# Kernel tuning notes

Measured on AMD Instinct MI355X. Metric: run time of the kernel, lower is better.

The kernel has to match this reference:

```python
import jax, jax.numpy as jnp
import numpy as np

B = 4096        # graphs
N0 = 32         # nodes per graph
N = B * N0      # 131072 nodes
EP = 128        # edges per graph
E = B * EP      # 524288 edges
H, C = 2, 64    # heads, per-head channels
D = H * C       # 128
K1, K2, K3 = 29, 27, 25  # ceil(0.9*32), ceil(0.9*29), ceil(0.9*27)


def setup_inputs() -> dict:
    key = jax.random.key(0)
    ks = jax.random.split(key, 8)
    x = jax.random.normal(ks[0], (N, 41), jnp.float32)
    g = jnp.repeat(jnp.arange(B, dtype=jnp.int32), EP)
    src = g * N0 + jax.random.randint(ks[1], (E,), 0, N0, jnp.int32)
    dst = g * N0 + jax.random.randint(ks[2], (E,), 0, N0, jnp.int32)
    edge_index = jnp.stack([src, dst])
    edge_attr = jax.random.normal(ks[3], (E, 10), jnp.float32)
    batch = jnp.repeat(jnp.arange(B, dtype=jnp.int32), N0)

    def lin(k, i, o):
        return jax.random.normal(k, (i, o), jnp.float32) / np.float32(np.sqrt(i))

    p = {"x": x, "edge_index": edge_index, "edge_attr": edge_attr, "batch": batch}
    fins = {1: 41, 2: D, 3: D}
    for li in (1, 2, 3):
        sub = jax.random.split(ks[3 + li], 6)
        p[f"W{li}"] = lin(sub[0], fins[li], D)
        p[f"We{li}"] = lin(sub[1], 10, D)
        p[f"as{li}"] = jax.random.normal(sub[2], (H, C), jnp.float32) * 0.1
        p[f"ad{li}"] = jax.random.normal(sub[3], (H, C), jnp.float32) * 0.1
        p[f"ae{li}"] = jax.random.normal(sub[4], (H, C), jnp.float32) * 0.1
        p[f"b{li}"] = jnp.zeros((D,), jnp.float32)
        p[f"g{li}"] = jnp.ones((D,), jnp.float32)
        p[f"be{li}"] = jnp.zeros((D,), jnp.float32)
        p[f"pw{li}"] = jax.random.normal(sub[5], (D,), jnp.float32)
    sub = jax.random.split(ks[7], 2)
    p["fw1"] = lin(sub[0], D, 64)
    p["fb1"] = jnp.zeros((64,), jnp.float32)
    p["fw2"] = lin(sub[1], 64, 1)
    p["fb2"] = jnp.zeros((1,), jnp.float32)
    return p


def gat_conv(x, src, dst, edge_attr, node_mask, edge_mask, W, We, a_s, a_d, a_e, b):
    # PyG GATConv w/ edge_dim, add_self_loops=True, fill_value='mean'
    emf = edge_mask.astype(x.dtype)
    loop_attr = jax.ops.segment_sum(edge_attr * emf[:, None], dst, num_segments=N)
    loop_attr = loop_attr / jnp.maximum(jax.ops.segment_sum(emf, dst, num_segments=N), 1.0)[:, None]
    idx = jnp.arange(N, dtype=src.dtype)
    s = jnp.concatenate([src, idx])
    d = jnp.concatenate([dst, idx])
    ea = jnp.concatenate([edge_attr, loop_attr], axis=0)
    msk = jnp.concatenate([edge_mask, node_mask])
    h = (x @ W).reshape(N, H, C)                       # [N,H,C]
    eh = (ea @ We).reshape(-1, H, C)                   # [E+N,H,C]
    alpha = (h * a_s).sum(-1)[s] + (h * a_d).sum(-1)[d] + (eh * a_e).sum(-1)
    alpha = jax.nn.leaky_relu(alpha, 0.2)              # [E+N,H]
    alpha = jnp.where(msk[:, None], alpha, -1e9)
    mx = jax.ops.segment_max(alpha, d, num_segments=N)  # segment softmax over dst
    p = jnp.where(msk[:, None], jnp.exp(alpha - mx[d]), 0.0)
    den = jax.ops.segment_sum(p, d, num_segments=N)
    w = p / jnp.maximum(den[d], 1e-16)
    out = jax.ops.segment_sum(w[:, :, None] * h[s], d, num_segments=N)
    return out.reshape(N, D) + b


def masked_bn(x, nm, gamma, beta, eps=1e-5):
    m = nm.astype(x.dtype)[:, None]
    n = jnp.maximum(m.sum(), 1.0)
    mu = (x * m).sum(0) / n
    var = (jnp.square(x - mu) * m).sum(0) / n
    return gamma * (x - mu) * jax.lax.rsqrt(var + eps) + beta


def topk_pool(x, w, nm, k):
    sc = (x @ w) / jnp.linalg.norm(w)                  # [N]
    sg = jnp.where(nm, sc, -1e9).reshape(B, N0)
    _, idx = jax.lax.top_k(sg, k)                      # per-graph top-k
    nm2 = jnp.zeros((B, N0), bool).at[jnp.arange(B)[:, None], idx].set(True).reshape(-1)
    xn = jnp.where(nm2[:, None], x * jnp.tanh(sc)[:, None], 0.0)
    return xn, nm2


def graph_mean(x, nm, batch):
    m = nm.astype(x.dtype)
    s = jax.ops.segment_sum(x * m[:, None], batch, num_segments=B)
    c = jax.ops.segment_sum(m, batch, num_segments=B)
    return s / jnp.maximum(c, 1.0)[:, None]


def _forward(x, edge_index, edge_attr, batch,
             W1, We1, as1, ad1, ae1, b1, g1, be1, pw1,
             W2, We2, as2, ad2, ae2, b2, g2, be2, pw2,
             W3, We3, as3, ad3, ae3, b3, g3, be3, pw3,
             fw1, fb1, fw2, fb2):
    src, dst = edge_index[0], edge_index[1]
    nm = jnp.ones((N,), bool)
    em = jnp.ones((E,), bool)
    layers = [(W1, We1, as1, ad1, ae1, b1, g1, be1, pw1, K1),
              (W2, We2, as2, ad2, ae2, b2, g2, be2, pw2, K2),
              (W3, We3, as3, ad3, ae3, b3, g3, be3, pw3, K3)]
    reads = []
    for (W, We, a_s, a_d, a_e, b, g, be, pw, k) in layers:
        x = gat_conv(x, src, dst, edge_attr, nm, em, W, We, a_s, a_d, a_e, b)
        x = jax.nn.relu(masked_bn(x, nm, g, be))
        x, nm = topk_pool(x, pw, nm, k)
        em = em & nm[src] & nm[dst]
        reads.append(graph_mean(x, nm, batch))
    z = reads[0] + reads[1] + reads[2]
    z = jax.nn.relu(z @ fw1 + fb1)
    return z @ fw2 + fb2


def reference(x, edge_index, edge_attr, batch,
              W1, We1, as1, ad1, ae1, b1, g1, be1, pw1,
              W2, We2, as2, ad2, ae2, b2, g2, be2, pw2,
              W3, We3, as3, ad3, ae3, b3, g3, be3, pw3,
              fw1, fb1, fw2, fb2):
    return _forward(x, edge_index, edge_attr, batch,
                    W1, We1, as1, ad1, ae1, b1, g1, be1, pw1,
                    W2, We2, as2, ad2, ae2, b2, g2, be2, pw2,
                    W3, We3, as3, ad3, ae3, b3, g3, be3, pw3,
                    fw1, fb1, fw2, fb2)
```

## Files before the change

### kernel.cpp

```cpp
#include <hip/hip_runtime.h>

#define NN 131072
#define NG 4096
#define NE 524288

__device__ __forceinline__ float lrelu(float a){ return a>=0.f ? a : 0.2f*a; }

template<int K, int PMODE, int KSEL>
__global__ __launch_bounds__(256) void pool_gemm_kernel(
    const float* __restrict__ Xin, float* bufA, unsigned char* nmg,
    const float* __restrict__ stat,
    const float* __restrict__ gamma, const float* __restrict__ beta,
    const float* __restrict__ Wg,
    float* zacc)
{
    constexpr int XP = (K == 41) ? 44 : 132;
    __shared__ float xs[64 * XP];
    __shared__ float scS[64], tsS[64];
    __shared__ int   nmlS[64];

    int tid = threadIdx.x;
    long row0 = (long)blockIdx.x * 64;
    int g0 = blockIdx.x * 2;

    if (PMODE == 0) {
        for (int i = tid; i < 64 * 41; i += 256) {
            int r = i / 41, c = i - r * 41;
            xs[r * 44 + c] = Xin[row0 * 41 + i];
        }
    } else {
        for (int i = tid; i < 2048; i += 256) {
            int r = i >> 5, dc = (i & 31) * 4;
            float4 v = *(const float4*)&bufA[(row0 + r) * 128 + dc];
            v.x = fmaxf(gamma[dc    ] * (v.x - stat[dc    ]) * stat[128 + dc    ] + beta[dc    ], 0.f);
            v.y = fmaxf(gamma[dc + 1] * (v.y - stat[dc + 1]) * stat[128 + dc + 1] + beta[dc + 1], 0.f);
            v.z = fmaxf(gamma[dc + 2] * (v.z - stat[dc + 2]) * stat[128 + dc + 2] + beta[dc + 2], 0.f);
            v.w = fmaxf(gamma[dc + 3] * (v.w - stat[dc + 3]) * stat[128 + dc + 3] + beta[dc + 3], 0.f);
            *(float4*)&xs[r * XP + dc] = v;
        }
        if (tid < 64) nmlS[tid] = (PMODE == 1) ? 1 : (int)nmg[g0 * 32 + tid];
    }
    __syncthreads();

    if (PMODE > 0) {
        {
            int node = tid >> 2, l4 = tid & 3;
            float s = 0.f;
            for (int m = 0; m < 32; m++) { int c = l4 + 4 * m; s += xs[node * XP + c] * stat[256 + c]; }
            s += __shfl_xor(s, 2); s += __shfl_xor(s, 1);
            if (l4 == 0) scS[node] = s;
        }
        __syncthreads();
        if (tid < 64) {
            int gp = tid >> 5, n = tid & 31;
            float sn = nmlS[tid] ? scS[tid] : -1e9f;
            int cnt = 0;
            for (int j = 0; j < 32; j++) {
                float sj = nmlS[gp * 32 + j] ? scS[gp * 32 + j] : -1e9f;
                cnt += (sj > sn || (sj == sn && j < n)) ? 1 : 0;
            }
            int sl = (cnt < KSEL) ? 1 : 0;
            nmg[g0 * 32 + tid] = (unsigned char)sl;
            tsS[tid] = sl ? tanhf(scS[tid]) : 0.f;
        }
        __syncthreads();
        for (int i = tid; i < 2048; i += 256) {
            int r = i >> 5, dc = (i & 31) * 4;
            float t = tsS[r];
            float4 v = *(const float4*)&xs[r * XP + dc];
            v.x *= t; v.y *= t; v.z *= t; v.w *= t;
            *(float4*)&xs[r * XP + dc] = v;
        }
        __syncthreads();
        {
            int gp = tid >> 7, d = tid & 127;
            float s = 0.f;
            for (int n = 0; n < 32; n++) s += xs[(gp * 32 + n) * XP + d];
            zacc[(long)(g0 + gp) * 128 + d] += s * (1.0f / (float)KSEL);
        }
        __syncthreads();
    }

    int r0 = (tid >> 5) * 8, c4 = (tid & 31) * 4;
    float acc[8][4];
#pragma unroll
    for (int i = 0; i < 8; i++)
#pragma unroll
        for (int j = 0; j < 4; j++) acc[i][j] = 0.f;

    constexpr int KM4 = (K / 4) * 4;
#pragma unroll 2
    for (int k0 = 0; k0 < KM4; k0 += 4) {
        float4 wv0 = *(const float4*)&Wg[(k0 + 0) * 128 + c4];
        float4 wv1 = *(const float4*)&Wg[(k0 + 1) * 128 + c4];
        float4 wv2 = *(const float4*)&Wg[(k0 + 2) * 128 + c4];
        float4 wv3 = *(const float4*)&Wg[(k0 + 3) * 128 + c4];
#pragma unroll
        for (int i = 0; i < 8; i++) {
            float4 xv = *(const float4*)&xs[(r0 + i) * XP + k0];
            acc[i][0] += xv.x * wv0.x + xv.y * wv1.x + xv.z * wv2.x + xv.w * wv3.x;
            acc[i][1] += xv.x * wv0.y + xv.y * wv1.y + xv.z * wv2.y + xv.w * wv3.y;
            acc[i][2] += xv.x * wv0.z + xv.y * wv1.z + xv.z * wv2.z + xv.w * wv3.z;
            acc[i][3] += xv.x * wv0.w + xv.y * wv1.w + xv.z * wv2.w + xv.w * wv3.w;
        }
    }
    for (int k = KM4; k < K; k++) {
        float4 wv = *(const float4*)&Wg[k * 128 + c4];
#pragma unroll
        for (int i = 0; i < 8; i++) {
            float xv = xs[(r0 + i) * XP + k];
            acc[i][0] += xv * wv.x; acc[i][1] += xv * wv.y;
            acc[i][2] += xv * wv.z; acc[i][3] += xv * wv.w;
        }
    }
#pragma unroll
    for (int i = 0; i < 8; i++)
        *(float4*)&bufA[(row0 + r0 + i) * 128 + c4] =
            make_float4(acc[i][0], acc[i][1], acc[i][2], acc[i][3]);
}

__global__ __launch_bounds__(256) void attn_kernel(
    float* bufA,
    const int* __restrict__ srcp, const int* __restrict__ dstp,
    const float* __restrict__ EA,
    const unsigned char* __restrict__ nmg,
    const float* __restrict__ stat,
    const float* __restrict__ as_, const float* __restrict__ ad_,
    const float* __restrict__ bb,
    float* sums)
{
    __shared__ float hs[32 * 128];
    __shared__ float Wm[2 * 32 * 36];
    __shared__ float scr[320];
    __shared__ unsigned char nmlS[32];

    int g = blockIdx.x, tid = threadIdx.x;
    long gb = (long)g * 4096;

    float ea0 = 0.f, ea1 = 0.f;
    int myls = 0, myld = 0;
    if (tid < 128) {
        myls = srcp[g * 128 + tid] & 31;
        myld = dstp[g * 128 + tid] & 31;
        const float* ep = EA + (long)(g * 128 + tid) * 10;
#pragma unroll
        for (int j = 0; j < 10; j++) { float v = ep[j]; ea0 += v * stat[384 + j]; ea1 += v * stat[394 + j]; }
    }
    for (int i = tid; i < 2304; i += 256) Wm[i] = 0.f;
    if (tid < 96) scr[128 + tid] = 0.f;
    if (tid < 32) nmlS[tid] = nmg[g * 32 + tid];
#pragma unroll
    for (int k = 0; k < 4; k++) {
        int i = tid + 256 * k, r = i >> 5, c4 = i & 31;
        *(float4*)&hs[r * 128 + ((c4 ^ (r & 7)) << 2)] =
            *(const float4*)&bufA[gb + (long)i * 4];
    }
    __syncthreads();

    {
        int node = tid >> 3, l8 = tid & 7, rb = node * 128, k = node & 7;
        float s0 = 0, s1 = 0, d0 = 0, d1 = 0;
#pragma unroll
        for (int m = 0; m < 8; m++) {
            int c = l8 + 8 * m, c4 = c >> 2, j = c & 3;
            int o0 = rb + ((c4 ^ k) << 2) + j;
            float h0 = hs[o0], h1 = hs[o0 + 64];
            s0 += h0 * as_[c];      s1 += h1 * as_[64 + c];
            d0 += h0 * ad_[c];      d1 += h1 * ad_[64 + c];
        }
        s0 += __shfl_xor(s0, 4); s0 += __shfl_xor(s0, 2); s0 += __shfl_xor(s0, 1);
        s1 += __shfl_xor(s1, 4); s1 += __shfl_xor(s1, 2); s1 += __shfl_xor(s1, 1);
        d0 += __shfl_xor(d0, 4); d0 += __shfl_xor(d0, 2); d0 += __shfl_xor(d0, 1);
        d1 += __shfl_xor(d1, 4); d1 += __shfl_xor(d1, 2); d1 += __shfl_xor(d1, 1);
        if (l8 == 0) {
            scr[node * 2] = s0;      scr[node * 2 + 1] = s1;
            scr[64 + node * 2] = d0; scr[64 + node * 2 + 1] = d1;
        }
    }
    int mymk = 0;
    if (tid < 128) {
        mymk = (int)nmlS[myls] & (int)nmlS[myld];
        if (mymk) {
            atomicAdd(&scr[128 + myld * 2], ea0);
            atomicAdd(&scr[128 + myld * 2 + 1], ea1);
            atomicAdd(&scr[192 + myld], 1.f);
        }
    }
    __syncthreads();

    if (tid < 128) {
        if (mymk) {
            float p0 = __expf(lrelu(scr[myls * 2]     + scr[64 + myld * 2]     + ea0));
            float p1 = __expf(lrelu(scr[myls * 2 + 1] + scr[64 + myld * 2 + 1] + ea1));
            atomicAdd(&Wm[myls * 36 + myld], p0);
            atomicAdd(&Wm[1152 + myls * 36 + myld], p1);
        }
    } else if (tid < 192) {
        int t2 = tid - 128, n = t2 >> 1, h = t2 & 1;
        if (nmlS[n]) {
            float c = scr[192 + n]; c = (c > 0.f) ? c : 1.f;
            float ps = __expf(lrelu(scr[n * 2 + h] + scr[64 + n * 2 + h] + scr[128 + n * 2 + h] / c));
            atomicAdd(&Wm[h * 1152 + n * 36 + n], ps);
        }
    }
    __syncthreads();

    if (tid < 64) {
        int n = tid & 31, h = tid >> 5;
        const float* Wh = &Wm[h * 1152 + n];
        float den = 0.f;
#pragma unroll 8
        for (int s = 0; s < 32; s++) den += Wh[s * 36];
        scr[256 + h * 32 + n] = 1.f / fmaxf(den, 1e-16f);
    } else if (tid < 128) {
        *(float4*)&scr[(tid - 64) * 4] = make_float4(0.f, 0.f, 0.f, 0.f);
    }
    __syncthreads();

    {
        int d = tid & 127, h = d >> 6, nb = tid >> 7;
        int c4 = d >> 2, j = d & 3;
        const float* Wh = &Wm[h * 1152 + nb * 16];
        float acc[16];
#pragma unroll
        for (int i = 0; i < 16; i++) acc[i] = 0.f;
        for (int s = 0; s < 32; s++) {
            float hv = hs[s * 128 + ((c4 ^ (s & 7)) << 2) + j];
            float4 w0 = *(const float4*)&Wh[s * 36];
            float4 w1 = *(const float4*)&Wh[s * 36 + 4];
            float4 w2 = *(const float4*)&Wh[s * 36 + 8];
            float4 w3 = *(const float4*)&Wh[s * 36 + 12];
            acc[0]  += w0.x * hv; acc[1]  += w0.y * hv; acc[2]  += w0.z * hv; acc[3]  += w0.w * hv;
            acc[4]  += w1.x * hv; acc[5]  += w1.y * hv; acc[6]  += w1.z * hv; acc[7]  += w1.w * hv;
            acc[8]  += w2.x * hv; acc[9]  += w2.y * hv; acc[10] += w2.z * hv; acc[11] += w2.w * hv;
            acc[12] += w3.x * hv; acc[13] += w3.y * hv; acc[14] += w3.z * hv; acc[15] += w3.w * hv;
        }
        float bv = bb[d];
        float sp = 0.f, sq = 0.f;
#pragma unroll
        for (int i = 0; i < 16; i++) {
            int n = nb * 16 + i;
            float v = acc[i] * scr[256 + h * 32 + n] + bv;
            bufA[gb + n * 128 + d] = v;
            if (nmlS[n]) { sp += v; sq += v * v; }
        }
        atomicAdd(&scr[d], sp);
        atomicAdd(&scr[128 + d], sq);
    }
    __syncthreads();

    if (tid < 128) {
        int rep = (g & 31) * 256;
        atomicAdd(&sums[rep + tid], scr[tid]);
        atomicAdd(&sums[rep + 128 + tid], scr[128 + tid]);
    }
}

__global__ __launch_bounds__(128) void setup_kernel(
    float* sums, float* stat, const float* __restrict__ We, const float* __restrict__ ae)
{
    int t = threadIdx.x;
    for (int i = t; i < 32 * 256; i += 128) sums[i] = 0.f;
    if (t < 20) {
        int h = t / 10, j = t - 10 * h;
        float s = 0.f;
        for (int c = 0; c < 64; c++) s += We[j * 128 + h * 64 + c] * ae[h * 64 + c];
        stat[384 + t] = s;
    }
}

__global__ __launch_bounds__(128) void finalize_kernel(
    float* sums, float n, const float* __restrict__ pw, float* stat,
    const float* __restrict__ Wen, const float* __restrict__ aen)
{
    int d = threadIdx.x;
    float s1 = 0.f, s2 = 0.f;
#pragma unroll
    for (int r = 0; r < 32; r++) { s1 += sums[r * 256 + d]; s2 += sums[r * 256 + 128 + d]; }
    float mean = s1 / n;
    float var = s2 / n - mean * mean;
    if (var < 0.f) var = 0.f;
    float rstd = rsqrtf(var + 1e-5f);
    float p = pw[d];
    float q = p * p;
#pragma unroll
    for (int o = 32; o >= 1; o >>= 1) q += __shfl_xor(q, o);
    __shared__ float w2[2];
    if ((d & 63) == 0) w2[d >> 6] = q;
    __syncthreads();
    float nrm = sqrtf(w2[0] + w2[1]);
    stat[d] = mean; stat[128 + d] = rstd; stat[256 + d] = p / nrm;
    if (d < 20) {
        int h = d / 10, j = d - 10 * h;
        float s = 0.f;
        for (int c = 0; c < 64; c++) s += Wen[j * 128 + h * 64 + c] * aen[h * 64 + c];
        stat[384 + d] = s;
    }
    for (int i = d; i < 32 * 256; i += 128) sums[i] = 0.f;
}

__global__ __launch_bounds__(256) void final_kernel(
    const float* __restrict__ bufA, const unsigned char* __restrict__ nmg,
    const float* __restrict__ stat,
    const float* __restrict__ gamma, const float* __restrict__ beta,
    const float* __restrict__ zacc,
    const float* __restrict__ fw1, const float* __restrict__ fb1,
    const float* __restrict__ fw2, const float* __restrict__ fb2,
    float* __restrict__ out)
{
    __shared__ float xs[32 * 132], zt[128], hred[64], scS[32], tsS[32];
    __shared__ int nmlS[32];
    int g = blockIdx.x, tid = threadIdx.x;
    long gb = (long)g * 4096;

    if (tid < 32) nmlS[tid] = (int)nmg[g * 32 + tid];
    for (int i = tid; i < 1024; i += 256) {
        int r = i >> 5, dc = (i & 31) * 4;
        float4 v = *(const float4*)&bufA[gb + i * 4];
        v.x = fmaxf(gamma[dc    ] * (v.x - stat[dc    ]) * stat[128 + dc    ] + beta[dc    ], 0.f);
        v.y = fmaxf(gamma[dc + 1] * (v.y - stat[dc + 1]) * stat[128 + dc + 1] + beta[dc + 1], 0.f);
        v.z = fmaxf(gamma[dc + 2] * (v.z - stat[dc + 2]) * stat[128 + dc + 2] + beta[dc + 2], 0.f);
        v.w = fmaxf(gamma[dc + 3] * (v.w - stat[dc + 3]) * stat[128 + dc + 3] + beta[dc + 3], 0.f);
        *(float4*)&xs[r * 132 + dc] = v;
    }
    __syncthreads();

    {
        int node = tid >> 3, l8 = tid & 7;
        float s = 0.f;
        for (int m = 0; m < 16; m++) { int c = l8 + 8 * m; s += xs[node * 132 + c] * stat[256 + c]; }
        s += __shfl_xor(s, 4); s += __shfl_xor(s, 2); s += __shfl_xor(s, 1);
        if (l8 == 0) scS[node] = s;
    }
    __syncthreads();

    if (tid < 32) {
        float sn = nmlS[tid] ? scS[tid] : -1e9f;
        int cnt = 0;
        for (int j = 0; j < 32; j++) {
            float sj = nmlS[j] ? scS[j] : -1e9f;
            cnt += (sj > sn || (sj == sn && j < tid)) ? 1 : 0;
        }
        tsS[tid] = (cnt < 25) ? tanhf(scS[tid]) : 0.f;
    }
    __syncthreads();

    if (tid < 128) {
        float s = 0.f;
        for (int n = 0; n < 32; n++) s += xs[n * 132 + tid] * tsS[n];
        zt[tid] = zacc[(long)g * 128 + tid] + s * (1.0f / 25.0f);
    }
    __syncthreads();

    {
        int j = tid >> 2, p = tid & 3;
        float s = 0.f;
        for (int d = p * 32; d < p * 32 + 32; d++) s += zt[d] * fw1[d * 64 + j];
        s += __shfl_xor(s, 1); s += __shfl_xor(s, 2);
        if (p == 0) hred[j] = fmaxf(s + fb1[j], 0.f) * fw2[j];
    }
    __syncthreads();
    if (tid < 64) {
        float v = hred[tid];
#pragma unroll
        for (int o = 32; o >= 1; o >>= 1) v += __shfl_xor(v, o);
        if (tid == 0) out[g] = v + fb2[0];
    }
}

extern "C" void kernel_launch(void* const* d_in, const int* in_sizes, int n_in,
                              void* d_out, int out_size, void* d_ws, size_t ws_size,
                              hipStream_t stream)
{
    const float* X0 = (const float*)d_in[0];
    const int*   EI = (const int*)d_in[1];
    const float* EA = (const float*)d_in[2];
    const int* srcp = EI;
    const int* dstp = EI + NE;

    const float* W1  = (const float*)d_in[4];  const float* We1 = (const float*)d_in[5];
    const float* as1 = (const float*)d_in[6];  const float* ad1 = (const float*)d_in[7];
    const float* ae1 = (const float*)d_in[8];  const float* b1  = (const float*)d_in[9];
    const float* g1  = (const float*)d_in[10]; const float* be1 = (const float*)d_in[11];
    const float* pw1 = (const float*)d_in[12];
    const float* W2  = (const float*)d_in[13]; const float* We2 = (const float*)d_in[14];
    const float* as2 = (const float*)d_in[15]; const float* ad2 = (const float*)d_in[16];
    const float* ae2 = (const float*)d_in[17]; const float* b2  = (const float*)d_in[18];
    const float* g2  = (const float*)d_in[19]; const float* be2 = (const float*)d_in[20];
    const float* pw2 = (const float*)d_in[21];
    const float* W3  = (const float*)d_in[22]; const float* We3 = (const float*)d_in[23];
    const float* as3 = (const float*)d_in[24]; const float* ad3 = (const float*)d_in[25];
    const float* ae3 = (const float*)d_in[26]; const float* b3  = (const float*)d_in[27];
    const float* g3  = (const float*)d_in[28]; const float* be3 = (const float*)d_in[29];
    const float* pw3 = (const float*)d_in[30];
    const float* fw1 = (const float*)d_in[31]; const float* fb1 = (const float*)d_in[32];
    const float* fw2 = (const float*)d_in[33]; const float* fb2 = (const float*)d_in[34];

    float* bufA = (float*)d_ws;
    float* z    = bufA + (size_t)NN * 128;
    float* sums = z + (size_t)NG * 128;
    float* stat = sums + 32 * 256;
    unsigned char* nmg = (unsigned char*)(stat + 512);

    hipMemsetAsync(nmg, 1, NN, stream);
    hipMemsetAsync(z, 0, (size_t)NG * 128 * sizeof(float), stream);
    setup_kernel<<<1, 128, 0, stream>>>(sums, stat, We1, ae1);

    pool_gemm_kernel<41, 0, 1><<<NN / 64, 256, 0, stream>>>(
        X0, bufA, nmg, stat, g1, be1, W1, z);
    attn_kernel<<<NG, 256, 0, stream>>>(bufA, srcp, dstp, EA, nmg, stat, as1, ad1, b1, sums);
    finalize_kernel<<<1, 128, 0, stream>>>(sums, 131072.f, pw1, stat, We2, ae2);

    pool_gemm_kernel<128, 1, 29><<<NN / 64, 256, 0, stream>>>(
        X0, bufA, nmg, stat, g1, be1, W2, z);
    attn_kernel<<<NG, 256, 0, stream>>>(bufA, srcp, dstp, EA, nmg, stat, as2, ad2, b2, sums);
    finalize_kernel<<<1, 128, 0, stream>>>(sums, 4096.f * 29.f, pw2, stat, We3, ae3);

    pool_gemm_kernel<128, 2, 27><<<NN / 64, 256, 0, stream>>>(
        X0, bufA, nmg, stat, g2, be2, W3, z);
    attn_kernel<<<NG, 256, 0, stream>>>(bufA, srcp, dstp, EA, nmg, stat, as3, ad3, b3, sums);
    finalize_kernel<<<1, 128, 0, stream>>>(sums, 4096.f * 27.f, pw3, stat, We3, ae3);

    final_kernel<<<NG, 256, 0, stream>>>(
        bufA, nmg, stat, g3, be3, z, fw1, fb1, fw2, fb2, (float*)d_out);
}
```

Baseline: 533.8 us.

## Fuse pool/GEMM and attention kernels into one per-layer kernel

Merges the pooling+linear-projection kernel with the GAT attention/aggregation kernel so each block of 64 nodes (two graphs) projects features into shared memory and then performs attention and aggregation without writing and rereading the projected features through global memory. The shared feature tile is switched to an XOR-swizzled 128-wide layout, and the attention stage now handles two graphs per block. This removes one kernel launch per layer and a full round trip of the node feature buffer, at the cost of higher shared memory use per block (about 56KB), which may lower occupancy.

```diff
diff --git a/kernel.cpp b/kernel.cpp
--- a/kernel.cpp
+++ b/kernel.cpp
@@ -7,21 +7,42 @@
 __device__ __forceinline__ float lrelu(float a){ return a>=0.f ? a : 0.2f*a; }
 
 template<int K, int PMODE, int KSEL>
-__global__ __launch_bounds__(256) void pool_gemm_kernel(
+__global__ __launch_bounds__(256) void layer_kernel(
     const float* __restrict__ Xin, float* bufA, unsigned char* nmg,
     const float* __restrict__ stat,
     const float* __restrict__ gamma, const float* __restrict__ beta,
     const float* __restrict__ Wg,
-    float* zacc)
+    float* zacc,
+    const int* __restrict__ srcp, const int* __restrict__ dstp,
+    const float* __restrict__ EA,
+    const float* __restrict__ as_, const float* __restrict__ ad_,
+    const float* __restrict__ bb,
+    float* sums)
 {
-    constexpr int XP = (K == 41) ? 44 : 132;
-    __shared__ float xs[64 * XP];
+    __shared__ float xs[64 * 128];
+    __shared__ float Wm[4608];
+    __shared__ float scr[576];
     __shared__ float scS[64], tsS[64];
-    __shared__ int   nmlS[64];
+    __shared__ unsigned char nmlS[64];
 
     int tid = threadIdx.x;
     long row0 = (long)blockIdx.x * 64;
     int g0 = blockIdx.x * 2;
+
+    int eid = g0 * 128 + tid;
+    int myls = srcp[eid] & 31, myld = dstp[eid] & 31;
+    int gph = tid >> 7;
+    int ls64 = gph * 32 + myls, ld64 = gph * 32 + myld;
+    float ea0 = 0.f, ea1 = 0.f;
+    {
+        const float* ep = EA + (long)eid * 10;
+#pragma unroll
+        for (int j = 0; j < 10; j++) { float v = ep[j]; ea0 += v * stat[384 + j]; ea1 += v * stat[394 + j]; }
+    }
+
+    for (int i = tid; i < 4608; i += 256) Wm[i] = 0.f;
+    if (tid < 192) scr[256 + tid] = 0.f;
+    if (tid < 64) nmlS[tid] = (PMODE == 2) ? nmg[g0 * 32 + tid] : (unsigned char)1;
 
     if (PMODE == 0) {
         for (int i = tid; i < 64 * 41; i += 256) {
@@ -30,27 +51,28 @@
         }
     } else {
         for (int i = tid; i < 2048; i += 256) {
-            int r = i >> 5, dc = (i & 31) * 4;
+            int r = i >> 5, c4 = i & 31, dc = c4 * 4;
             float4 v = *(const float4*)&bufA[(row0 + r) * 128 + dc];
             v.x = fmaxf(gamma[dc    ] * (v.x - stat[dc    ]) * stat[128 + dc    ] + beta[dc    ], 0.f);
             v.y = fmaxf(gamma[dc + 1] * (v.y - stat[dc + 1]) * stat[128 + dc + 1] + beta[dc + 1], 0.f);
             v.z = fmaxf(gamma[dc + 2] * (v.z - stat[dc + 2]) * stat[128 + dc + 2] + beta[dc + 2], 0.f);
             v.w = fmaxf(gamma[dc + 3] * (v.w - stat[dc + 3]) * stat[128 + dc + 3] + beta[dc + 3], 0.f);
-            *(float4*)&xs[r * XP + dc] = v;
-        }
-        if (tid < 64) nmlS[tid] = (PMODE == 1) ? 1 : (int)nmg[g0 * 32 + tid];
+            *(float4*)&xs[r * 128 + ((c4 ^ (r & 7)) << 2)] = v;
+        }
     }
     __syncthreads();
 
     if (PMODE > 0) {
         {
-            int node = tid >> 2, l4 = tid & 3;
+            int node = tid >> 2, l4 = tid & 3, kk = node & 7;
             float s = 0.f;
-            for (int m = 0; m < 32; m++) { int c = l4 + 4 * m; s += xs[node * XP + c] * stat[256 + c]; }
+            for (int m = 0; m < 32; m++)
+                s += xs[node * 128 + (((m ^ kk)) << 2) + l4] * stat[256 + 4 * m + l4];
             s += __shfl_xor(s, 2); s += __shfl_xor(s, 1);
             if (l4 == 0) scS[node] = s;
         }
         __syncthreads();
+        int sl = 0;
         if (tid < 64) {
             int gp = tid >> 5, n = tid & 31;
             float sn = nmlS[tid] ? scS[tid] : -1e9f;
@@ -59,29 +81,35 @@
                 float sj = nmlS[gp * 32 + j] ? scS[gp * 32 + j] : -1e9f;
                 cnt += (sj > sn || (sj == sn && j < n)) ? 1 : 0;
             }
-            int sl = (cnt < KSEL) ? 1 : 0;
+            sl = (cnt < KSEL) ? 1 : 0;
+        }
+        __syncthreads();
+        if (tid < 64) {
             nmg[g0 * 32 + tid] = (unsigned char)sl;
+            nmlS[tid] = (unsigned char)sl;
             tsS[tid] = sl ? tanhf(scS[tid]) : 0.f;
         }
         __syncthreads();
         for (int i = tid; i < 2048; i += 256) {
-            int r = i >> 5, dc = (i & 31) * 4;
+            int r = i >> 5, c4 = i & 31;
             float t = tsS[r];
-            float4 v = *(const float4*)&xs[r * XP + dc];
+            float4* p = (float4*)&xs[r * 128 + ((c4 ^ (r & 7)) << 2)];
+            float4 v = *p;
             v.x *= t; v.y *= t; v.z *= t; v.w *= t;
-            *(float4*)&xs[r * XP + dc] = v;
+            *p = v;
         }
         __syncthreads();
         {
-            int gp = tid >> 7, d = tid & 127;
+            int gp = tid >> 7, d = tid & 127, c4 = d >> 2, j = d & 3;
             float s = 0.f;
-            for (int n = 0; n < 32; n++) s += xs[(gp * 32 + n) * XP + d];
+            for (int n = 0; n < 32; n++)
+                s += xs[(gp * 32 + n) * 128 + ((c4 ^ (n & 7)) << 2) + j];
             zacc[(long)(g0 + gp) * 128 + d] += s * (1.0f / (float)KSEL);
         }
         __syncthreads();
     }
 
-    int r0 = (tid >> 5) * 8, c4 = (tid & 31) * 4;
+    int r0 = (tid >> 5) * 8, c4w = (tid & 31) * 4;
     float acc[8][4];
 #pragma unroll
     for (int i = 0; i < 8; i++)
@@ -91,13 +119,16 @@
     constexpr int KM4 = (K / 4) * 4;
 #pragma unroll 2
     for (int k0 = 0; k0 < KM4; k0 += 4) {
-        float4 wv0 = *(const float4*)&Wg[(k0 + 0) * 128 + c4];
-        float4 wv1 = *(const float4*)&Wg[(k0 + 1) * 128 + c4];
-        float4 wv2 = *(const float4*)&Wg[(k0 + 2) * 128 + c4];
-        float4 wv3 = *(const float4*)&Wg[(k0 + 3) * 128 + c4];
+        float4 wv0 = *(const float4*)&Wg[(k0 + 0) * 128 + c4w];
+        float4 wv1 = *(const float4*)&Wg[(k0 + 1) * 128 + c4w];
+        float4 wv2 = *(const float4*)&Wg[(k0 + 2) * 128 + c4w];
+        float4 wv3 = *(const float4*)&Wg[(k0 + 3) * 128 + c4w];
 #pragma unroll
         for (int i = 0; i < 8; i++) {
-            float4 xv = *(const float4*)&xs[(r0 + i) * XP + k0];
+            int r = r0 + i;
+            float4 xv = (PMODE == 0)
+                ? *(const float4*)&xs[r * 44 + k0]
+                : *(const float4*)&xs[r * 128 + ((((k0 >> 2) ^ (r & 7))) << 2)];
             acc[i][0] += xv.x * wv0.x + xv.y * wv1.x + xv.z * wv2.x + xv.w * wv3.x;
             acc[i][1] += xv.x * wv0.y + xv.y * wv1.y + xv.z * wv2.y + xv.w * wv3.y;
             acc[i][2] += xv.x * wv0.z + xv.y * wv1.z + xv.z * wv2.z + xv.w * wv3.z;
@@ -105,152 +136,120 @@
         }
     }
     for (int k = KM4; k < K; k++) {
-        float4 wv = *(const float4*)&Wg[k * 128 + c4];
+        float4 wv = *(const float4*)&Wg[k * 128 + c4w];
 #pragma unroll
         for (int i = 0; i < 8; i++) {
-            float xv = xs[(r0 + i) * XP + k];
+            float xv = (PMODE == 0) ? xs[(r0 + i) * 44 + k]
+                                    : xs[(r0 + i) * 128 + (((k >> 2) ^ ((r0 + i) & 7)) << 2) + (k & 3)];
             acc[i][0] += xv * wv.x; acc[i][1] += xv * wv.y;
             acc[i][2] += xv * wv.z; acc[i][3] += xv * wv.w;
         }
     }
-#pragma unroll
-    for (int i = 0; i < 8; i++)
-        *(float4*)&bufA[(row0 + r0 + i) * 128 + c4] =
-            make_float4(acc[i][0], acc[i][1], acc[i][2], acc[i][3]);
-}
-
-__global__ __launch_bounds__(256) void attn_kernel(
-    float* bufA,
-    const int* __restrict__ srcp, const int* __restrict__ dstp,
-    const float* __restrict__ EA,
-    const unsigned char* __restrict__ nmg,
-    const float* __restrict__ stat,
-    const float* __restrict__ as_, const float* __restrict__ ad_,
-    const float* __restrict__ bb,
-    float* sums)
-{
-    __shared__ float hs[32 * 128];
-    __shared__ float Wm[2 * 32 * 36];
-    __shared__ float scr[320];
-    __shared__ unsigned char nmlS[32];
-
-    int g = blockIdx.x, tid = threadIdx.x;
-    long gb = (long)g * 4096;
-
-    float ea0 = 0.f, ea1 = 0.f;
-    int myls = 0, myld = 0;
-    if (tid < 128) {
-        myls = srcp[g * 128 + tid] & 31;
-        myld = dstp[g * 128 + tid] & 31;
-        const float* ep = EA + (long)(g * 128 + tid) * 10;
-#pragma unroll
-        for (int j = 0; j < 10; j++) { float v = ep[j]; ea0 += v * stat[384 + j]; ea1 += v * stat[394 + j]; }
-    }
-    for (int i = tid; i < 2304; i += 256) Wm[i] = 0.f;
-    if (tid < 96) scr[128 + tid] = 0.f;
-    if (tid < 32) nmlS[tid] = nmg[g * 32 + tid];
-#pragma unroll
-    for (int k = 0; k < 4; k++) {
-        int i = tid + 256 * k, r = i >> 5, c4 = i & 31;
-        *(float4*)&hs[r * 128 + ((c4 ^ (r & 7)) << 2)] =
-            *(const float4*)&bufA[gb + (long)i * 4];
-    }
-    __syncthreads();
-
-    {
-        int node = tid >> 3, l8 = tid & 7, rb = node * 128, k = node & 7;
+    __syncthreads();
+    {
+        int cc = tid & 31;
+#pragma unroll
+        for (int i = 0; i < 8; i++) {
+            int r = r0 + i;
+            *(float4*)&xs[r * 128 + ((cc ^ (r & 7)) << 2)] =
+                make_float4(acc[i][0], acc[i][1], acc[i][2], acc[i][3]);
+        }
+    }
+    __syncthreads();
+
+    {
+        int node = tid >> 2, l4 = tid & 3, kk = node & 7, rb = node * 128;
         float s0 = 0, s1 = 0, d0 = 0, d1 = 0;
 #pragma unroll
-        for (int m = 0; m < 8; m++) {
-            int c = l8 + 8 * m, c4 = c >> 2, j = c & 3;
-            int o0 = rb + ((c4 ^ k) << 2) + j;
-            float h0 = hs[o0], h1 = hs[o0 + 64];
+        for (int m = 0; m < 16; m++) {
+            int c = l4 + 4 * m;
+            int o = rb + ((m ^ kk) << 2) + l4;
+            float h0 = xs[o], h1 = xs[o + 64];
             s0 += h0 * as_[c];      s1 += h1 * as_[64 + c];
             d0 += h0 * ad_[c];      d1 += h1 * ad_[64 + c];
         }
-        s0 += __shfl_xor(s0, 4); s0 += __shfl_xor(s0, 2); s0 += __shfl_xor(s0, 1);
-        s1 += __shfl_xor(s1, 4); s1 += __shfl_xor(s1, 2); s1 += __shfl_xor(s1, 1);
-        d0 += __shfl_xor(d0, 4); d0 += __shfl_xor(d0, 2); d0 += __shfl_xor(d0, 1);
-        d1 += __shfl_xor(d1, 4); d1 += __shfl_xor(d1, 2); d1 += __shfl_xor(d1, 1);
-        if (l8 == 0) {
-            scr[node * 2] = s0;      scr[node * 2 + 1] = s1;
-            scr[64 + node * 2] = d0; scr[64 + node * 2 + 1] = d1;
-        }
-    }
-    int mymk = 0;
+        s0 += __shfl_xor(s0, 2); s0 += __shfl_xor(s0, 1);
+        s1 += __shfl_xor(s1, 2); s1 += __shfl_xor(s1, 1);
+        d0 += __shfl_xor(d0, 2); d0 += __shfl_xor(d0, 1);
+        d1 += __shfl_xor(d1, 2); d1 += __shfl_xor(d1, 1);
+        if (l4 == 0) {
+            scr[node * 2] = s0;       scr[node * 2 + 1] = s1;
+            scr[128 + node * 2] = d0; scr[128 + node * 2 + 1] = d1;
+        }
+    }
+    int mymk = (int)nmlS[ls64] & (int)nmlS[ld64];
+    if (mymk) {
+        atomicAdd(&scr[256 + ld64 * 2], ea0);
+        atomicAdd(&scr[256 + ld64 * 2 + 1], ea1);
+        atomicAdd(&scr[384 + ld64], 1.f);
+    }
+    __syncthreads();
+
+    if (mymk) {
+        float p0 = __expf(lrelu(scr[ls64 * 2]     + scr[128 + ld64 * 2]     + ea0));
+        float p1 = __expf(lrelu(scr[ls64 * 2 + 1] + scr[128 + ld64 * 2 + 1] + ea1));
+        atomicAdd(&Wm[gph * 2304 + myls * 36 + myld], p0);
+        atomicAdd(&Wm[gph * 2304 + 1152 + myls * 36 + myld], p1);
+    }
     if (tid < 128) {
-        mymk = (int)nmlS[myls] & (int)nmlS[myld];
-        if (mymk) {
-            atomicAdd(&scr[128 + myld * 2], ea0);
-            atomicAdd(&scr[128 + myld * 2 + 1], ea1);
-            atomicAdd(&scr[192 + myld], 1.f);
+        int n64 = tid >> 1, hh = tid & 1, gp = n64 >> 5, n = n64 & 31;
+        if (nmlS[n64]) {
+            float c = scr[384 + n64]; c = (c > 0.f) ? c : 1.f;
+            float ps = __expf(lrelu(scr[n64 * 2 + hh] + scr[128 + n64 * 2 + hh] + scr[256 + n64 * 2 + hh] / c));
+            atomicAdd(&Wm[gp * 2304 + hh * 1152 + n * 36 + n], ps);
         }
     }
     __syncthreads();
 
     if (tid < 128) {
-        if (mymk) {
-            float p0 = __expf(lrelu(scr[myls * 2]     + scr[64 + myld * 2]     + ea0));
-            float p1 = __expf(lrelu(scr[myls * 2 + 1] + scr[64 + myld * 2 + 1] + ea1));
-            atomicAdd(&Wm[myls * 36 + myld], p0);
-            atomicAdd(&Wm[1152 + myls * 36 + myld], p1);
-        }
-    } else if (tid < 192) {
-        int t2 = tid - 128, n = t2 >> 1, h = t2 & 1;
-        if (nmlS[n]) {
-            float c = scr[192 + n]; c = (c > 0.f) ? c : 1.f;
-            float ps = __expf(lrelu(scr[n * 2 + h] + scr[64 + n * 2 + h] + scr[128 + n * 2 + h] / c));
-            atomicAdd(&Wm[h * 1152 + n * 36 + n], ps);
-        }
-    }
-    __syncthreads();
-
-    if (tid < 64) {
-        int n = tid & 31, h = tid >> 5;
-        const float* Wh = &Wm[h * 1152 + n];
+        int gp = tid >> 6, hh = (tid >> 5) & 1, n = tid & 31;
+        const float* Wh = &Wm[gp * 2304 + hh * 1152 + n];
         float den = 0.f;
 #pragma unroll 8
         for (int s = 0; s < 32; s++) den += Wh[s * 36];
-        scr[256 + h * 32 + n] = 1.f / fmaxf(den, 1e-16f);
-    } else if (tid < 128) {
-        *(float4*)&scr[(tid - 64) * 4] = make_float4(0.f, 0.f, 0.f, 0.f);
-    }
-    __syncthreads();
-
-    {
-        int d = tid & 127, h = d >> 6, nb = tid >> 7;
-        int c4 = d >> 2, j = d & 3;
-        const float* Wh = &Wm[h * 1152 + nb * 16];
-        float acc[16];
-#pragma unroll
-        for (int i = 0; i < 16; i++) acc[i] = 0.f;
-        for (int s = 0; s < 32; s++) {
-            float hv = hs[s * 128 + ((c4 ^ (s & 7)) << 2) + j];
-            float4 w0 = *(const float4*)&Wh[s * 36];
-            float4 w1 = *(const float4*)&Wh[s * 36 + 4];
-            float4 w2 = *(const float4*)&Wh[s * 36 + 8];
-            float4 w3 = *(const float4*)&Wh[s * 36 + 12];
-            acc[0]  += w0.x * hv; acc[1]  += w0.y * hv; acc[2]  += w0.z * hv; acc[3]  += w0.w * hv;
-            acc[4]  += w1.x * hv; acc[5]  += w1.y * hv; acc[6]  += w1.z * hv; acc[7]  += w1.w * hv;
-            acc[8]  += w2.x * hv; acc[9]  += w2.y * hv; acc[10] += w2.z * hv; acc[11] += w2.w * hv;
-            acc[12] += w3.x * hv; acc[13] += w3.y * hv; acc[14] += w3.z * hv; acc[15] += w3.w * hv;
-        }
+        scr[448 + (gp * 32 + n) * 2 + hh] = 1.f / fmaxf(den, 1e-16f);
+    } else {
+        int t = (tid - 128) * 2;
+        scr[t] = 0.f; scr[t + 1] = 0.f;
+    }
+    __syncthreads();
+
+    {
+        int d = tid & 127, hh = d >> 6, nb = tid >> 7, c4 = d >> 2, j = d & 3;
         float bv = bb[d];
-        float sp = 0.f, sq = 0.f;
-#pragma unroll
-        for (int i = 0; i < 16; i++) {
-            int n = nb * 16 + i;
-            float v = acc[i] * scr[256 + h * 32 + n] + bv;
-            bufA[gb + n * 128 + d] = v;
-            if (nmlS[n]) { sp += v; sq += v * v; }
-        }
-        atomicAdd(&scr[d], sp);
-        atomicAdd(&scr[128 + d], sq);
+        float spT = 0.f, sqT = 0.f;
+#pragma unroll
+        for (int gp = 0; gp < 2; gp++) {
+            const float* Wh = &Wm[gp * 2304 + hh * 1152 + nb * 16];
+            float a2[16];
+#pragma unroll
+            for (int i = 0; i < 16; i++) a2[i] = 0.f;
+            for (int s = 0; s < 32; s++) {
+                float hv = xs[(gp * 32 + s) * 128 + ((c4 ^ (s & 7)) << 2) + j];
+                float4 w0 = *(const float4*)&Wh[s * 36];
+                float4 w1 = *(const float4*)&Wh[s * 36 + 4];
+                float4 w2 = *(const float4*)&Wh[s * 36 + 8];
+                float4 w3 = *(const float4*)&Wh[s * 36 + 12];
+                a2[0]  += w0.x * hv; a2[1]  += w0.y * hv; a2[2]  += w0.z * hv; a2[3]  += w0.w * hv;
+                a2[4]  += w1.x * hv; a2[5]  += w1.y * hv; a2[6]  += w1.z * hv; a2[7]  += w1.w * hv;
+                a2[8]  += w2.x * hv; a2[9]  += w2.y * hv; a2[10] += w2.z * hv; a2[11] += w2.w * hv;
+                a2[12] += w3.x * hv; a2[13] += w3.y * hv; a2[14] += w3.z * hv; a2[15] += w3.w * hv;
+            }
+#pragma unroll
+            for (int i = 0; i < 16; i++) {
+                int n = nb * 16 + i;
+                float v = a2[i] * scr[448 + (gp * 32 + n) * 2 + hh] + bv;
+                bufA[(long)(g0 + gp) * 4096 + n * 128 + d] = v;
+                if (nmlS[gp * 32 + n]) { spT += v; sqT += v * v; }
+            }
+        }
+        atomicAdd(&scr[d], spT);
+        atomicAdd(&scr[128 + d], sqT);
     }
     __syncthreads();
 
     if (tid < 128) {
-        int rep = (g & 31) * 256;
+        int rep = (blockIdx.x & 31) * 256;
         atomicAdd(&sums[rep + tid], scr[tid]);
         atomicAdd(&sums[rep + 128 + tid], scr[128 + tid]);
     }
@@ -406,19 +405,16 @@
     hipMemsetAsync(z, 0, (size_t)NG * 128 * sizeof(float), stream);
     setup_kernel<<<1, 128, 0, stream>>>(sums, stat, We1, ae1);
 
-    pool_gemm_kernel<41, 0, 1><<<NN / 64, 256, 0, stream>>>(
-        X0, bufA, nmg, stat, g1, be1, W1, z);
-    attn_kernel<<<NG, 256, 0, stream>>>(bufA, srcp, dstp, EA, nmg, stat, as1, ad1, b1, sums);
+    layer_kernel<41, 0, 1><<<NN / 64, 256, 0, stream>>>(
+        X0, bufA, nmg, stat, g1, be1, W1, z, srcp, dstp, EA, as1, ad1, b1, sums);
     finalize_kernel<<<1, 128, 0, stream>>>(sums, 131072.f, pw1, stat, We2, ae2);
 
-    pool_gemm_kernel<128, 1, 29><<<NN / 64, 256, 0, stream>>>(
-        X0, bufA, nmg, stat, g1, be1, W2, z);
-    attn_kernel<<<NG, 256, 0, stream>>>(bufA, srcp, dstp, EA, nmg, stat, as2, ad2, b2, sums);
+    layer_kernel<128, 1, 29><<<NN / 64, 256, 0, stream>>>(
+        X0, bufA, nmg, stat, g1, be1, W2, z, srcp, dstp, EA, as2, ad2, b2, sums);
     finalize_kernel<<<1, 128, 0, stream>>>(sums, 4096.f * 29.f, pw2, stat, We3, ae3);
 
-    pool_gemm_kernel<128, 2, 27><<<NN / 64, 256, 0, stream>>>(
-        X0, bufA, nmg, stat, g2, be2, W3, z);
-    attn_kernel<<<NG, 256, 0, stream>>>(bufA, srcp, dstp, EA, nmg, stat, as3, ad3, b3, sums);
+    layer_kernel<128, 2, 27><<<NN / 64, 256, 0, stream>>>(
+        X0, bufA, nmg, stat, g2, be2, W3, z, srcp, dstp, EA, as3, ad3, b3, sums);
     finalize_kernel<<<1, 128, 0, stream>>>(sums, 4096.f * 27.f, pw3, stat, We3, ae3);
 
     final_kernel<<<NG, 256, 0, stream>>>(
```

Measured after the change: 569.1 us. 6.6% more time.

## Fuse pooling/GEMM kernel into attention kernel, one graph per block

Applied to the files above, without the earlier changes.

Merges the per-layer pool+GEMM kernel and the attention kernel into a single layer kernel launched with one block per graph. The projected features stay in shared memory (swizzled layout) rather than being written to global memory and read back. The tanh pooling scale is now applied to the GEMM outputs instead of scaling the inputs beforehand. This removes one kernel launch and one full global round trip of the 131072x128 feature buffer per layer. In exchange each block does a smaller 32-row GEMM with fewer accumulators per thread, and shared-memory use per block is higher.

```diff
diff --git a/kernel.cpp b/kernel.cpp
--- a/kernel.cpp
+++ b/kernel.cpp
@@ -7,129 +7,20 @@
 __device__ __forceinline__ float lrelu(float a){ return a>=0.f ? a : 0.2f*a; }
 
 template<int K, int PMODE, int KSEL>
-__global__ __launch_bounds__(256) void pool_gemm_kernel(
+__global__ __launch_bounds__(256) void layer_kernel(
     const float* __restrict__ Xin, float* bufA, unsigned char* nmg,
     const float* __restrict__ stat,
     const float* __restrict__ gamma, const float* __restrict__ beta,
     const float* __restrict__ Wg,
-    float* zacc)
-{
-    constexpr int XP = (K == 41) ? 44 : 132;
-    __shared__ float xs[64 * XP];
-    __shared__ float scS[64], tsS[64];
-    __shared__ int   nmlS[64];
-
-    int tid = threadIdx.x;
-    long row0 = (long)blockIdx.x * 64;
-    int g0 = blockIdx.x * 2;
-
-    if (PMODE == 0) {
-        for (int i = tid; i < 64 * 41; i += 256) {
-            int r = i / 41, c = i - r * 41;
-            xs[r * 44 + c] = Xin[row0 * 41 + i];
-        }
-    } else {
-        for (int i = tid; i < 2048; i += 256) {
-            int r = i >> 5, dc = (i & 31) * 4;
-            float4 v = *(const float4*)&bufA[(row0 + r) * 128 + dc];
-            v.x = fmaxf(gamma[dc    ] * (v.x - stat[dc    ]) * stat[128 + dc    ] + beta[dc    ], 0.f);
-            v.y = fmaxf(gamma[dc + 1] * (v.y - stat[dc + 1]) * stat[128 + dc + 1] + beta[dc + 1], 0.f);
-            v.z = fmaxf(gamma[dc + 2] * (v.z - stat[dc + 2]) * stat[128 + dc + 2] + beta[dc + 2], 0.f);
-            v.w = fmaxf(gamma[dc + 3] * (v.w - stat[dc + 3]) * stat[128 + dc + 3] + beta[dc + 3], 0.f);
-            *(float4*)&xs[r * XP + dc] = v;
-        }
-        if (tid < 64) nmlS[tid] = (PMODE == 1) ? 1 : (int)nmg[g0 * 32 + tid];
-    }
-    __syncthreads();
-
-    if (PMODE > 0) {
-        {
-            int node = tid >> 2, l4 = tid & 3;
-            float s = 0.f;
-            for (int m = 0; m < 32; m++) { int c = l4 + 4 * m; s += xs[node * XP + c] * stat[256 + c]; }
-            s += __shfl_xor(s, 2); s += __shfl_xor(s, 1);
-            if (l4 == 0) scS[node] = s;
-        }
-        __syncthreads();
-        if (tid < 64) {
-            int gp = tid >> 5, n = tid & 31;
-            float sn = nmlS[tid] ? scS[tid] : -1e9f;
-            int cnt = 0;
-            for (int j = 0; j < 32; j++) {
-                float sj = nmlS[gp * 32 + j] ? scS[gp * 32 + j] : -1e9f;
-                cnt += (sj > sn || (sj == sn && j < n)) ? 1 : 0;
-            }
-            int sl = (cnt < KSEL) ? 1 : 0;
-            nmg[g0 * 32 + tid] = (unsigned char)sl;
-            tsS[tid] = sl ? tanhf(scS[tid]) : 0.f;
-        }
-        __syncthreads();
-        for (int i = tid; i < 2048; i += 256) {
-            int r = i >> 5, dc = (i & 31) * 4;
-            float t = tsS[r];
-            float4 v = *(const float4*)&xs[r * XP + dc];
-            v.x *= t; v.y *= t; v.z *= t; v.w *= t;
-            *(float4*)&xs[r * XP + dc] = v;
-        }
-        __syncthreads();
-        {
-            int gp = tid >> 7, d = tid & 127;
-            float s = 0.f;
-            for (int n = 0; n < 32; n++) s += xs[(gp * 32 + n) * XP + d];
-            zacc[(long)(g0 + gp) * 128 + d] += s * (1.0f / (float)KSEL);
-        }
-        __syncthreads();
-    }
-
-    int r0 = (tid >> 5) * 8, c4 = (tid & 31) * 4;
-    float acc[8][4];
-#pragma unroll
-    for (int i = 0; i < 8; i++)
-#pragma unroll
-        for (int j = 0; j < 4; j++) acc[i][j] = 0.f;
-
-    constexpr int KM4 = (K / 4) * 4;
-#pragma unroll 2
-    for (int k0 = 0; k0 < KM4; k0 += 4) {
-        float4 wv0 = *(const float4*)&Wg[(k0 + 0) * 128 + c4];
-        float4 wv1 = *(const float4*)&Wg[(k0 + 1) * 128 + c4];
-        float4 wv2 = *(const float4*)&Wg[(k0 + 2) * 128 + c4];
-        float4 wv3 = *(const float4*)&Wg[(k0 + 3) * 128 + c4];
-#pragma unroll
-        for (int i = 0; i < 8; i++) {
-            float4 xv = *(const float4*)&xs[(r0 + i) * XP + k0];
-            acc[i][0] += xv.x * wv0.x + xv.y * wv1.x + xv.z * wv2.x + xv.w * wv3.x;
-            acc[i][1] += xv.x * wv0.y + xv.y * wv1.y + xv.z * wv2.y + xv.w * wv3.y;
-            acc[i][2] += xv.x * wv0.z + xv.y * wv1.z + xv.z * wv2.z + xv.w * wv3.z;
-            acc[i][3] += xv.x * wv0.w + xv.y * wv1.w + xv.z * wv2.w + xv.w * wv3.w;
-        }
-    }
-    for (int k = KM4; k < K; k++) {
-        float4 wv = *(const float4*)&Wg[k * 128 + c4];
-#pragma unroll
-        for (int i = 0; i < 8; i++) {
-            float xv = xs[(r0 + i) * XP + k];
-            acc[i][0] += xv * wv.x; acc[i][1] += xv * wv.y;
-            acc[i][2] += xv * wv.z; acc[i][3] += xv * wv.w;
-        }
-    }
-#pragma unroll
-    for (int i = 0; i < 8; i++)
-        *(float4*)&bufA[(row0 + r0 + i) * 128 + c4] =
-            make_float4(acc[i][0], acc[i][1], acc[i][2], acc[i][3]);
-}
-
-__global__ __launch_bounds__(256) void attn_kernel(
-    float* bufA,
+    float* zacc,
     const int* __restrict__ srcp, const int* __restrict__ dstp,
     const float* __restrict__ EA,
-    const unsigned char* __restrict__ nmg,
-    const float* __restrict__ stat,
     const float* __restrict__ as_, const float* __restrict__ ad_,
     const float* __restrict__ bb,
     float* sums)
 {
     __shared__ float hs[32 * 128];
+    __shared__ float xin[(K == 41) ? 32 * 44 : 4];
     __shared__ float Wm[2 * 32 * 36];
     __shared__ float scr[320];
     __shared__ unsigned char nmlS[32];
@@ -137,8 +28,8 @@
     int g = blockIdx.x, tid = threadIdx.x;
     long gb = (long)g * 4096;
 
+    int myls = 0, myld = 0;
     float ea0 = 0.f, ea1 = 0.f;
-    int myls = 0, myld = 0;
     if (tid < 128) {
         myls = srcp[g * 128 + tid] & 31;
         myld = dstp[g * 128 + tid] & 31;
@@ -146,24 +37,126 @@
 #pragma unroll
         for (int j = 0; j < 10; j++) { float v = ep[j]; ea0 += v * stat[384 + j]; ea1 += v * stat[394 + j]; }
     }
+
     for (int i = tid; i < 2304; i += 256) Wm[i] = 0.f;
     if (tid < 96) scr[128 + tid] = 0.f;
-    if (tid < 32) nmlS[tid] = nmg[g * 32 + tid];
-#pragma unroll
-    for (int k = 0; k < 4; k++) {
-        int i = tid + 256 * k, r = i >> 5, c4 = i & 31;
-        *(float4*)&hs[r * 128 + ((c4 ^ (r & 7)) << 2)] =
-            *(const float4*)&bufA[gb + (long)i * 4];
-    }
-    __syncthreads();
-
+    if (tid < 32) nmlS[tid] = (PMODE == 2) ? nmg[g * 32 + tid] : (unsigned char)1;
+
+    if (PMODE == 0) {
+        for (int i = tid; i < 32 * 41; i += 256) {
+            int r = i / 41, c = i - r * 41;
+            xin[r * 44 + c] = Xin[(long)g * 32 * 41 + i];
+        }
+    } else {
+        for (int i = tid; i < 1024; i += 256) {
+            int r = i >> 5, c4 = i & 31, dc = c4 * 4;
+            float4 v = *(const float4*)&bufA[gb + (long)i * 4];
+            v.x = fmaxf(gamma[dc    ] * (v.x - stat[dc    ]) * stat[128 + dc    ] + beta[dc    ], 0.f);
+            v.y = fmaxf(gamma[dc + 1] * (v.y - stat[dc + 1]) * stat[128 + dc + 1] + beta[dc + 1], 0.f);
+            v.z = fmaxf(gamma[dc + 2] * (v.z - stat[dc + 2]) * stat[128 + dc + 2] + beta[dc + 2], 0.f);
+            v.w = fmaxf(gamma[dc + 3] * (v.w - stat[dc + 3]) * stat[128 + dc + 3] + beta[dc + 3], 0.f);
+            *(float4*)&hs[r * 128 + ((c4 ^ (r & 7)) << 2)] = v;
+        }
+    }
+    __syncthreads();
+
+    if (PMODE > 0) {
+        {
+            int node = tid >> 3, l8 = tid & 7, kk = node & 7, rb = node * 128;
+            float s = 0.f;
+#pragma unroll
+            for (int m = 0; m < 16; m++) {
+                int c = l8 + 8 * m, c4 = c >> 2, j = c & 3;
+                s += hs[rb + ((c4 ^ kk) << 2) + j] * stat[256 + c];
+            }
+            s += __shfl_xor(s, 4); s += __shfl_xor(s, 2); s += __shfl_xor(s, 1);
+            if (l8 == 0) scr[256 + node] = s;
+        }
+        __syncthreads();
+        if (tid < 32) {
+            float sn = nmlS[tid] ? scr[256 + tid] : -1e9f;
+            int cnt = 0;
+            for (int j = 0; j < 32; j++) {
+                float sj = nmlS[j] ? scr[256 + j] : -1e9f;
+                cnt += (sj > sn || (sj == sn && j < tid)) ? 1 : 0;
+            }
+            int sl = (cnt < KSEL) ? 1 : 0;
+            nmg[g * 32 + tid] = (unsigned char)sl;
+            nmlS[tid] = (unsigned char)sl;
+            scr[288 + tid] = sl ? tanhf(scr[256 + tid]) : 0.f;
+        }
+        __syncthreads();
+        if (tid < 128) {
+            int d = tid, c4 = d >> 2, j = d & 3;
+            float s = 0.f;
+            for (int n = 0; n < 32; n++)
+                s += scr[288 + n] * hs[n * 128 + ((c4 ^ (n & 7)) << 2) + j];
+            zacc[(long)g * 128 + d] += s * (1.0f / (float)KSEL);
+        }
+    }
+
+    int r0 = (tid >> 5) * 4, c4w = (tid & 31) * 4;
+    float acc[4][4];
+#pragma unroll
+    for (int i = 0; i < 4; i++)
+#pragma unroll
+        for (int j = 0; j < 4; j++) acc[i][j] = 0.f;
+
+    constexpr int KM4 = (K / 4) * 4;
+#pragma unroll 2
+    for (int k0 = 0; k0 < KM4; k0 += 4) {
+        float4 wv0 = *(const float4*)&Wg[(k0 + 0) * 128 + c4w];
+        float4 wv1 = *(const float4*)&Wg[(k0 + 1) * 128 + c4w];
+        float4 wv2 = *(const float4*)&Wg[(k0 + 2) * 128 + c4w];
+        float4 wv3 = *(const float4*)&Wg[(k0 + 3) * 128 + c4w];
+#pragma unroll
+        for (int i = 0; i < 4; i++) {
+            int r = r0 + i;
+            float4 xv = (PMODE == 0)
+                ? *(const float4*)&xin[r * 44 + k0]
+                : *(const float4*)&hs[r * 128 + ((((k0 >> 2) ^ (r & 7))) << 2)];
+            acc[i][0] += xv.x * wv0.x + xv.y * wv1.x + xv.z * wv2.x + xv.w * wv3.x;
+            acc[i][1] += xv.x * wv0.y + xv.y * wv1.y + xv.z * wv2.y + xv.w * wv3.y;
+            acc[i][2] += xv.x * wv0.z + xv.y * wv1.z + xv.z * wv2.z + xv.w * wv3.z;
+            acc[i][3] += xv.x * wv0.w + xv.y * wv1.w + xv.z * wv2.w + xv.w * wv3.w;
+        }
+    }
+    for (int k = KM4; k < K; k++) {
+        float4 wv = *(const float4*)&Wg[k * 128 + c4w];
+#pragma unroll
+        for (int i = 0; i < 4; i++) {
+            float xv = (PMODE == 0) ? xin[(r0 + i) * 44 + k]
+                                    : hs[(r0 + i) * 128 + (((k >> 2) ^ ((r0 + i) & 7)) << 2) + (k & 3)];
+            acc[i][0] += xv * wv.x; acc[i][1] += xv * wv.y;
+            acc[i][2] += xv * wv.z; acc[i][3] += xv * wv.w;
+        }
+    }
+    if (PMODE > 0) {
+#pragma unroll
+        for (int i = 0; i < 4; i++) {
+            float t = scr[288 + r0 + i];
+            acc[i][0] *= t; acc[i][1] *= t; acc[i][2] *= t; acc[i][3] *= t;
+        }
+    }
+    __syncthreads();
     {
-        int node = tid >> 3, l8 = tid & 7, rb = node * 128, k = node & 7;
+        int cc = tid & 31;
+#pragma unroll
+        for (int i = 0; i < 4; i++) {
+            int r = r0 + i;
+            *(float4*)&hs[r * 128 + ((cc ^ (r & 7)) << 2)] =
+                make_float4(acc[i][0], acc[i][1], acc[i][2], acc[i][3]);
+        }
+    }
+    __syncthreads();
+
+    {
+        int node = tid >> 3, l8 = tid & 7, kk = node & 7, rb = node * 128;
         float s0 = 0, s1 = 0, d0 = 0, d1 = 0;
 #pragma unroll
         for (int m = 0; m < 8; m++) {
             int c = l8 + 8 * m, c4 = c >> 2, j = c & 3;
-            int o0 = rb + ((c4 ^ k) << 2) + j;
+            int o0 = rb + ((c4 ^ kk) << 2) + j;
             float h0 = hs[o0], h1 = hs[o0 + 64];
             s0 += h0 * as_[c];      s1 += h1 * as_[64 + c];
             d0 += h0 * ad_[c];      d1 += h1 * ad_[64 + c];
@@ -196,51 +189,50 @@
             atomicAdd(&Wm[1152 + myls * 36 + myld], p1);
         }
     } else if (tid < 192) {
-        int t2 = tid - 128, n = t2 >> 1, h = t2 & 1;
+        int t2 = tid - 128, n = t2 >> 1, hh = t2 & 1;
         if (nmlS[n]) {
             float c = scr[192 + n]; c = (c > 0.f) ? c : 1.f;
-            float ps = __expf(lrelu(scr[n * 2 + h] + scr[64 + n * 2 + h] + scr[128 + n * 2 + h] / c));
-            atomicAdd(&Wm[h * 1152 + n * 36 + n], ps);
+            float ps = __expf(lrelu(scr[n * 2 + hh] + scr[64 + n * 2 + hh] + scr[128 + n * 2 + hh] / c));
+            atomicAdd(&Wm[hh * 1152 + n * 36 + n], ps);
         }
     }
     __syncthreads();
 
     if (tid < 64) {
-        int n = tid & 31, h = tid >> 5;
-        const float* Wh = &Wm[h * 1152 + n];
+        int n = tid & 31, hh = tid >> 5;
+        const float* Wh = &Wm[hh * 1152 + n];
         float den = 0.f;
 #pragma unroll 8
         for (int s = 0; s < 32; s++) den += Wh[s * 36];
-        scr[256 + h * 32 + n] = 1.f / fmaxf(den, 1e-16f);
+        scr[256 + hh * 32 + n] = 1.f / fmaxf(den, 1e-16f);
     } else if (tid < 128) {
         *(float4*)&scr[(tid - 64) * 4] = make_float4(0.f, 0.f, 0.f, 0.f);
     }
     __syncthreads();
 
     {
-        int d = tid & 127, h = d >> 6, nb = tid >> 7;
-        int c4 = d >> 2, j = d & 3;
-        const float* Wh = &Wm[h * 1152 + nb * 16];
-        float acc[16];
-#pragma unroll
-        for (int i = 0; i < 16; i++) acc[i] = 0.f;
+        int d = tid & 127, hh = d >> 6, nb = tid >> 7, c4 = d >> 2, j = d & 3;
+        const float* Wh = &Wm[hh * 1152 + nb * 16];
+        float a2[16];
+#pragma unroll
+        for (int i = 0; i < 16; i++) a2[i] = 0.f;
         for (int s = 0; s < 32; s++) {
             float hv = hs[s * 128 + ((c4 ^ (s & 7)) << 2) + j];
             float4 w0 = *(const float4*)&Wh[s * 36];
             float4 w1 = *(const float4*)&Wh[s * 36 + 4];
             float4 w2 = *(const float4*)&Wh[s * 36 + 8];
             float4 w3 = *(const float4*)&Wh[s * 36 + 12];
-            acc[0]  += w0.x * hv; acc[1]  += w0.y * hv; acc[2]  += w0.z * hv; acc[3]  += w0.w * hv;
-            acc[4]  += w1.x * hv; acc[5]  += w1.y * hv; acc[6]  += w1.z * hv; acc[7]  += w1.w * hv;
-            acc[8]  += w2.x * hv; acc[9]  += w2.y * hv; acc[10] += w2.z * hv; acc[11] += w2.w * hv;
-            acc[12] += w3.x * hv; acc[13] += w3.y * hv; acc[14] += w3.z * hv; acc[15] += w3.w * hv;
+            a2[0]  += w0.x * hv; a2[1]  += w0.y * hv; a2[2]  += w0.z * hv; a2[3]  += w0.w * hv;
+            a2[4]  += w1.x * hv; a2[5]  += w1.y * hv; a2[6]  += w1.z * hv; a2[7]  += w1.w * hv;
+            a2[8]  += w2.x * hv; a2[9]  += w2.y * hv; a2[10] += w2.z * hv; a2[11] += w2.w * hv;
+            a2[12] += w3.x * hv; a2[13] += w3.y * hv; a2[14] += w3.z * hv; a2[15] += w3.w * hv;
         }
         float bv = bb[d];
         float sp = 0.f, sq = 0.f;
 #pragma unroll
         for (int i = 0; i < 16; i++) {
             int n = nb * 16 + i;
-            float v = acc[i] * scr[256 + h * 32 + n] + bv;
+            float v = a2[i] * scr[256 + hh * 32 + n] + bv;
             bufA[gb + n * 128 + d] = v;
             if (nmlS[n]) { sp += v; sq += v * v; }
         }
@@ -406,19 +398,16 @@
     hipMemsetAsync(z, 0, (size_t)NG * 128 * sizeof(float), stream);
     setup_kernel<<<1, 128, 0, stream>>>(sums, stat, We1, ae1);
 
-    pool_gemm_kernel<41, 0, 1><<<NN / 64, 256, 0, stream>>>(
-        X0, bufA, nmg, stat, g1, be1, W1, z);
-    attn_kernel<<<NG, 256, 0, stream>>>(bufA, srcp, dstp, EA, nmg, stat, as1, ad1, b1, sums);
+    layer_kernel<41, 0, 1><<<NG, 256, 0, stream>>>(
+        X0, bufA, nmg, stat, g1, be1, W1, z, srcp, dstp, EA, as1, ad1, b1, sums);
     finalize_kernel<<<1, 128, 0, stream>>>(sums, 131072.f, pw1, stat, We2, ae2);
 
-    pool_gemm_kernel<128, 1, 29><<<NN / 64, 256, 0, stream>>>(
-        X0, bufA, nmg, stat, g1, be1, W2, z);
-    attn_kernel<<<NG, 256, 0, stream>>>(bufA, srcp, dstp, EA, nmg, stat, as2, ad2, b2, sums);
+    layer_kernel<128, 1, 29><<<NG, 256, 0, stream>>>(
+        X0, bufA, nmg, stat, g1, be1, W2, z, srcp, dstp, EA, as2, ad2, b2, sums);
     finalize_kernel<<<1, 128, 0, stream>>>(sums, 4096.f * 29.f, pw2, stat, We3, ae3);
 
-    pool_gemm_kernel<128, 2, 27><<<NN / 64, 256, 0, stream>>>(
-        X0, bufA, nmg, stat, g2, be2, W3, z);
-    attn_kernel<<<NG, 256, 0, stream>>>(bufA, srcp, dstp, EA, nmg, stat, as3, ad3, b3, sums);
+    layer_kernel<128, 2, 27><<<NG, 256, 0, stream>>>(
+        X0, bufA, nmg, stat, g2, be2, W3, z, srcp, dstp, EA, as3, ad3, b3, sums);
     finalize_kernel<<<1, 128, 0, stream>>>(sums, 4096.f * 27.f, pw3, stat, We3, ae3);
 
     final_kernel<<<NG, 256, 0, stream>>>(
```

New measurement: 568.5 us. 6.5% more time.
